# Kernel tuning notes

Hardware: AMD Instinct MI355X
Metric: run time of the kernel (lower is better)

The kernel has to match this reference:

```python
import jax, jax.numpy as jnp
import numpy as np

B = 16384  # batch size
DN = ('NCHW', 'OIHW', 'NCHW')


def maxpool2(x):
    # 2x2 max pool, stride 2, VALID (matches nn.MaxPool2d(2, 2))
    return jax.lax.reduce_window(x, -jnp.inf, jax.lax.max,
                                 (1, 1, 2, 2), (1, 1, 2, 2), 'VALID')


def setup_inputs() -> dict:
    key = jax.random.key(0)
    ks = jax.random.split(key, 7)
    return {
        'x': jax.random.normal(ks[0], (B, 1, 32, 32), jnp.float32),
        'w1': jax.random.normal(ks[1], (6, 1, 5, 5), jnp.float32) * 0.1,
        'w2': jax.random.normal(ks[2], (16, 6, 5, 5), jnp.float32) * 0.1,
        'fw1': jax.random.normal(ks[3], (120, 400), jnp.float32) * 0.05,
        'fw2': jax.random.normal(ks[4], (84, 120), jnp.float32) * 0.05,
        'fc3_w': jax.random.normal(ks[5], (10, 84), jnp.float32) * 0.1,
        'fc3_b': jax.random.normal(ks[6], (10,), jnp.float32) * 0.1,
    }


def reference(x, w1, w2, fw1, fw2, fc3_w, fc3_b):
    # conv1 (no bias in StdConv2D) -> relu -> pool
    h = jax.lax.conv_general_dilated(x, w1, (1, 1), 'VALID', dimension_numbers=DN)
    h = maxpool2(jax.nn.relu(h))                      # [B,6,14,14]
    # conv2 -> relu -> pool
    h = jax.lax.conv_general_dilated(h, w2, (1, 1), 'VALID', dimension_numbers=DN)
    h = maxpool2(jax.nn.relu(h))                      # [B,16,5,5]
    h = h.reshape(h.shape[0], 400)                    # channel-major flatten, as torch view
    # StdFC layers: x @ W.T, no bias
    h = jax.nn.relu(h @ fw1.T)                        # [B,120]
    h = jax.nn.relu(h @ fw2.T)                        # [B,84]
    logits = h @ fc3_w.T + fc3_b                      # nn.Linear fc3 with bias
    return jax.nn.softmax(logits, axis=1)
```

## Files before the change

kernel.cpp:

```cpp
#include <hip/hip_runtime.h>
#include <hip/hip_fp16.h>
#include <math.h>

#define TH 256

typedef __attribute__((ext_vector_type(8))) short short8;
typedef __attribute__((ext_vector_type(4))) float floatx4;

#define P1_S   0
#define X_S    9424
#define P2_S   9424
#define BT_S   12816
#define H1_S   12816
#define H2_S   13904
#define LOG_F  7368
#define W1B_U  7752
#define LDS_F  7904

static __device__ __forceinline__ unsigned short f2bf(float x) {
    union { float f; unsigned u; } v; v.f = x;
    return (unsigned short)((v.u + 0x7FFFu + ((v.u >> 16) & 1u)) >> 16);
}
static __device__ __forceinline__ __half2 uash2(unsigned u) {
    union { unsigned u; __half2 h; } v; v.u = u; return v.h;
}
static __device__ __forceinline__ unsigned bfpack(unsigned hi, unsigned lo) {
    return __builtin_amdgcn_perm(hi, lo, 0x07060302u);
}
static __device__ __forceinline__ short8 load_bf8t(const float* row, int kb, int K) {
    int b0 = (kb + 4 <= K) ? kb : (K - 8);
    int b1 = (kb + 8 <= K) ? (kb + 4) : (K - 8);
    uint4 w0 = *(const uint4*)(row + b0);
    uint4 w1 = *(const uint4*)(row + b1);
    union { int4 i; short8 s; } r;
    r.i.x = (int)bfpack(w0.y, w0.x);
    r.i.y = (int)bfpack(w0.w, w0.z);
    r.i.z = (int)bfpack(w1.y, w1.x);
    r.i.w = (int)bfpack(w1.w, w1.z);
    return r.s;
}

__global__ __launch_bounds__(TH) void lenet_kernel(
    const float* __restrict__ x,
    const float* __restrict__ w1,
    const float* __restrict__ w2g,
    const float* __restrict__ fw1,
    const float* __restrict__ fw2,
    const float* __restrict__ fc3w,
    const float* __restrict__ fc3b,
    float* __restrict__ out)
{
    __shared__ __align__(16) float sf[LDS_F];
    short* sh = (short*)sf;
    unsigned* su = (unsigned*)sf;
    const int* p1i = (const int*)sf;

    const int tid  = threadIdx.x;
    const int blk  = blockIdx.x;
    const int lane = tid & 63;
    const int wid  = tid >> 6;
    const int g    = lane >> 4;
    const int cn   = lane & 15;
    const int pr   = cn & 7;

    for (int sub = 0; sub < 3; ++sub) {
        const int nimg = (sub < 2) ? 3 : 2;
        const float4* xg = (const float4*)(x + ((size_t)blk * 8 + sub * 3) * 1024);
        for (int e = tid; e < nimg * 256; e += TH) {
            float4 v = xg[e];
            int m = e >> 8, rem = e & 255;
            int y = rem >> 3, k4 = rem & 7;
            int off = X_S + m * 1090 + y * 34 + k4 * 4;
            *(__half2*)(sh + off)     = __floats2half2_rn(v.x, v.y);
            *(__half2*)(sh + off + 2) = __floats2half2_rn(v.z, v.w);
        }
        if (sub == 0) {
            for (int e = tid; e < 150; e += TH) {
                __half h = __float2half(w1[e]);
                ((__half2*)(su + W1B_U))[e] = __half2half2(h);
            }
            for (int e = tid; e < 2560; e += TH) {
                int oc = e / 160, kk = e - oc * 160;
                int s = kk >> 5, r = kk & 31;
                float v = 0.f;
                if (r < 30) v = w2g[oc * 150 + (r % 6) * 25 + s * 5 + (r / 6)];
                sh[BT_S + oc * 168 + kk] = (short)f2bf(v);
            }
        }
        __syncthreads();

        const int ntask = nimg * 168;
        for (int t = tid; t < ntask; t += TH) {
            int m = t / 168, r = t - m * 168;
            int c = r % 6, q = r / 6;
            int i = q >> 1, hf = q & 1;
            const __half2* wb = (const __half2*)(su + W1B_U) + c * 25;
            const int xbase = X_S + m * 1090 + hf * 14;

            __half2 acc0[7], acc1[7];
            #pragma unroll
            for (int j = 0; j < 7; ++j) { acc0[j] = uash2(0u); acc1[j] = uash2(0u); }
            __half2 wprev[5];
            #pragma unroll
            for (int tt = 0; tt < 6; ++tt) {
                unsigned u[9];
                const unsigned* rp = (const unsigned*)(sh + xbase + (2 * i + tt) * 34);
                #pragma unroll
                for (int qq = 0; qq < 9; ++qq) u[qq] = rp[qq];
                __half2 p0[9], p1[8];
                #pragma unroll
                for (int qq = 0; qq < 9; ++qq) p0[qq] = uash2(u[qq]);
                #pragma unroll
                for (int qq = 0; qq < 8; ++qq)
                    p1[qq] = uash2(__builtin_amdgcn_perm(u[qq + 1], u[qq], 0x05040302u));

                if (tt < 5) {
                    __half2 wc[5];
                    #pragma unroll
                    for (int kx = 0; kx < 5; ++kx) wc[kx] = wb[tt * 5 + kx];
                    #pragma unroll
                    for (int j = 0; j < 7; ++j) {
                        acc0[j] = __hfma2(p0[j],     wc[0], acc0[j]);
                        acc0[j] = __hfma2(p1[j],     wc[1], acc0[j]);
                        acc0[j] = __hfma2(p0[j + 1], wc[2], acc0[j]);
                        acc0[j] = __hfma2(p1[j + 1], wc[3], acc0[j]);
                        acc0[j] = __hfma2(p0[j + 2], wc[4], acc0[j]);
                    }
                    if (tt >= 1) {
                        #pragma unroll
                        for (int j = 0; j < 7; ++j) {
                            acc1[j] = __hfma2(p0[j],     wprev[0], acc1[j]);
                            acc1[j] = __hfma2(p1[j],     wprev[1], acc1[j]);
                            acc1[j] = __hfma2(p0[j + 1], wprev[2], acc1[j]);
                            acc1[j] = __hfma2(p1[j + 1], wprev[3], acc1[j]);
                            acc1[j] = __hfma2(p0[j + 2], wprev[4], acc1[j]);
                        }
                    }
                    #pragma unroll
                    for (int kx = 0; kx < 5; ++kx) wprev[kx] = wc[kx];
                } else {
                    #pragma unroll
                    for (int j = 0; j < 7; ++j) {
                        acc1[j] = __hfma2(p0[j],     wprev[0], acc1[j]);
                        acc1[j] = __hfma2(p1[j],     wprev[1], acc1[j]);
                        acc1[j] = __hfma2(p0[j + 1], wprev[2], acc1[j]);
                        acc1[j] = __hfma2(p1[j + 1], wprev[3], acc1[j]);
                        acc1[j] = __hfma2(p0[j + 2], wprev[4], acc1[j]);
                    }
                }
            }
            int gi = sub * 3 + m;
            short* dst = sh + P1_S + gi * 1178 + i * 84 + hf * 42 + c;
            #pragma unroll
            for (int j = 0; j < 7; ++j) {
                float a0l = __half2float(__low2half(acc0[j]));
                float a0h = __half2float(__high2half(acc0[j]));
                float a1l = __half2float(__low2half(acc1[j]));
                float a1h = __half2float(__high2half(acc1[j]));
                float v = fmaxf(fmaxf(fmaxf(a0l, a0h), fmaxf(a1l, a1h)), 0.f);
                dst[j * 6] = (short)f2bf(v);
            }
        }
        __syncthreads();
    }

    {
        short8 Breg[5];
        #pragma unroll
        for (int s = 0; s < 5; ++s)
            Breg[s] = *(const short8*)(sh + BT_S + cn * 168 + s * 32 + 8 * g);

        for (int e = tid; e < 8 * 24; e += TH) {
            int im = e / 24;
            sh[P2_S + im * 424 + 400 + (e - im * 24)] = 0;
        }

        for (int w = wid; w < 25; w += 4) {
            int i = w / 5, jx = w - 5 * i;
            floatx4 a00 = {0.f,0.f,0.f,0.f}, a01 = {0.f,0.f,0.f,0.f};
            floatx4 a10 = {0.f,0.f,0.f,0.f}, a11 = {0.f,0.f,0.f,0.f};
            #pragma unroll
            for (int s = 0; s < 5; ++s) {
                #pragma unroll
                for (int dy = 0; dy < 2; ++dy) {
                    #pragma unroll
                    for (int dx = 0; dx < 2; ++dx) {
                        int as = pr * 1178 + (2 * i + dy + s) * 84 + (2 * jx + dx) * 6 + 8 * g;
                        int ai = as >> 1;
                        union { int4 i4; short8 s8; } a;
                        a.i4.x = p1i[ai];     a.i4.y = p1i[ai + 1];
                        a.i4.z = p1i[ai + 2]; a.i4.w = p1i[ai + 3];
                        floatx4* acc = dy == 0 ? (dx == 0 ? &a00 : &a01)
                                               : (dx == 0 ? &a10 : &a11);
                        *acc = __builtin_amdgcn_mfma_f32_16x16x32_bf16(a.s8, Breg[s], *acc, 0, 0, 0);
                    }
                }
            }
            if (g < 2) {
                #pragma unroll
                for (int rg = 0; rg < 4; ++rg) {
                    float v = fmaxf(fmaxf(a00[rg], a01[rg]), fmaxf(a10[rg], a11[rg]));
                    v = fmaxf(v, 0.f);
                    int im = 4 * g + rg;
                    sh[P2_S + im * 424 + cn * 25 + i * 5 + jx] = (short)f2bf(v);
                }
            }
        }
    }
    __syncthreads();

    {
        for (int e = tid; e < 8 * 16; e += TH) {
            int im = e >> 4;
            sh[H1_S + im * 136 + 120 + (e & 15)] = 0;
        }
        for (int nt = wid; nt < 8; nt += 4) {
            floatx4 acc = {0.f,0.f,0.f,0.f};
            int n = nt * 16 + cn;
            const float* wrow = fw1 + (size_t)(n < 120 ? n : 119) * 400;
            for (int ks = 0; ks < 13; ++ks) {
                int kb = ks * 32 + 8 * g;
                short8 b = load_bf8t(wrow, kb, 400);
                short8 a = *(const short8*)(sh + P2_S + pr * 424 + kb);
                acc = __builtin_amdgcn_mfma_f32_16x16x32_bf16(a, b, acc, 0, 0, 0);
            }
            if (g < 2 && n < 120) {
                #pragma unroll
                for (int rg = 0; rg < 4; ++rg)
                    sh[H1_S + (4 * g + rg) * 136 + n] = (short)f2bf(fmaxf(acc[rg], 0.f));
            }
        }
    }
    __syncthreads();

    {
        for (int e = tid; e < 8 * 20; e += TH) {
            int im = e / 20;
            sh[H2_S + im * 104 + 84 + (e - im * 20)] = 0;
        }
        for (int nt = wid; nt < 6; nt += 4) {
            floatx4 acc = {0.f,0.f,0.f,0.f};
            int n = nt * 16 + cn;
            const float* wrow = fw2 + (size_t)(n < 84 ? n : 83) * 120;
            for (int ks = 0; ks < 4; ++ks) {
                int kb = ks * 32 + 8 * g;
                short8 b = load_bf8t(wrow, kb, 120);
                short8 a = *(const short8*)(sh + H1_S + pr * 136 + kb);
                acc = __builtin_amdgcn_mfma_f32_16x16x32_bf16(a, b, acc, 0, 0, 0);
            }
            if (g < 2 && n < 84) {
                #pragma unroll
                for (int rg = 0; rg < 4; ++rg)
                    sh[H2_S + (4 * g + rg) * 104 + n] = (short)f2bf(fmaxf(acc[rg], 0.f));
            }
        }
    }
    __syncthreads();

    if (wid == 0) {
        floatx4 acc = {0.f,0.f,0.f,0.f};
        int n = cn;
        const float* wrow = fc3w + (size_t)(n < 10 ? n : 9) * 84;
        for (int ks = 0; ks < 3; ++ks) {
            int kb = ks * 32 + 8 * g;
            short8 b = load_bf8t(wrow, kb, 84);
            short8 a = *(const short8*)(sh + H2_S + pr * 104 + kb);
            acc = __builtin_amdgcn_mfma_f32_16x16x32_bf16(a, b, acc, 0, 0, 0);
        }
        if (g < 2 && n < 10) {
            float bias = fc3b[n];
            #pragma unroll
            for (int rg = 0; rg < 4; ++rg)
                sf[LOG_F + (4 * g + rg) * 12 + n] = acc[rg] + bias;
        }
    }
    __syncthreads();

    if (tid < 8) {
        const float* lg = sf + LOG_F + tid * 12;
        float mx = lg[0];
        #pragma unroll
        for (int n = 1; n < 10; ++n) mx = fmaxf(mx, lg[n]);
        float e[10]; float sum = 0.f;
        #pragma unroll
        for (int n = 0; n < 10; ++n) { e[n] = expf(lg[n] - mx); sum += e[n]; }
        float inv = 1.f / sum;
        float* op = out + ((size_t)blk * 8 + tid) * 10;
        #pragma unroll
        for (int n = 0; n < 10; ++n) op[n] = e[n] * inv;
    }
}

extern "C" void kernel_launch(void* const* d_in, const int* in_sizes, int n_in,
                              void* d_out, int out_size, void* d_ws, size_t ws_size,
                              hipStream_t stream) {
    const float* x    = (const float*)d_in[0];
    const float* w1   = (const float*)d_in[1];
    const float* w2   = (const float*)d_in[2];
    const float* fw1  = (const float*)d_in[3];
    const float* fw2  = (const float*)d_in[4];
    const float* fc3w = (const float*)d_in[5];
    const float* fc3b = (const float*)d_in[6];
    float* outp = (float*)d_out;

    dim3 grid(16384 / 8), block(TH);
    hipLaunchKernelGGL(lenet_kernel, grid, block, 0, stream,
                       x, w1, w2, fw1, fw2, fc3w, fc3b, outp);
}
```

Before: 84.56 us.

## Prefetch next input batch into registers and halve conv2 MFMA count

Input images for the next sub-batch are loaded from global memory into registers while the current conv1 computes, and staging into LDS is done from those registers. A barrier moves to the start of each sub-iteration to protect the LDS buffer. Conv2 now packs both pooling rows (dy) into the M dimension of the MFMA using lanes 8-15, which halves the MFMA count. The two pooled rows are then reduced with a cross-lane shuffle. This adds register pressure and a shuffle in exchange for hidden load latency and fewer matrix instructions.

```diff
diff --git a/kernel.cpp b/kernel.cpp
--- a/kernel.cpp
+++ b/kernel.cpp
@@ -62,17 +62,28 @@
     const int g    = lane >> 4;
     const int cn   = lane & 15;
     const int pr   = cn & 7;
-
+    const int dyr  = cn >> 3;
+
+    float4 xreg[3];
+    {
+        const float4* xg0 = (const float4*)(x + (size_t)blk * 8 * 1024);
+        #pragma unroll
+        for (int j = 0; j < 3; ++j) { int e = tid + j * TH; if (e < 768) xreg[j] = xg0[e]; }
+    }
     for (int sub = 0; sub < 3; ++sub) {
         const int nimg = (sub < 2) ? 3 : 2;
-        const float4* xg = (const float4*)(x + ((size_t)blk * 8 + sub * 3) * 1024);
-        for (int e = tid; e < nimg * 256; e += TH) {
-            float4 v = xg[e];
-            int m = e >> 8, rem = e & 255;
-            int y = rem >> 3, k4 = rem & 7;
-            int off = X_S + m * 1090 + y * 34 + k4 * 4;
-            *(__half2*)(sh + off)     = __floats2half2_rn(v.x, v.y);
-            *(__half2*)(sh + off + 2) = __floats2half2_rn(v.z, v.w);
+        if (sub) __syncthreads();
+        #pragma unroll
+        for (int j = 0; j < 3; ++j) {
+            int e = tid + j * TH;
+            if (e < nimg * 256) {
+                float4 v = xreg[j];
+                int m = e >> 8, rem = e & 255;
+                int y = rem >> 3, k4 = rem & 7;
+                int off = X_S + m * 1090 + y * 34 + k4 * 4;
+                *(__half2*)(sh + off)     = __floats2half2_rn(v.x, v.y);
+                *(__half2*)(sh + off + 2) = __floats2half2_rn(v.z, v.w);
+            }
         }
         if (sub == 0) {
             for (int e = tid; e < 150; e += TH) {
@@ -88,6 +99,13 @@
             }
         }
         __syncthreads();
+
+        if (sub < 2) {
+            const int nimgn = (sub == 0) ? 3 : 2;
+            const float4* xgn = (const float4*)(x + ((size_t)blk * 8 + (sub + 1) * 3) * 1024);
+            #pragma unroll
+            for (int j = 0; j < 3; ++j) { int e = tid + j * TH; if (e < nimgn * 256) xreg[j] = xgn[e]; }
+        }
 
         const int ntask = nimg * 168;
         for (int t = tid; t < ntask; t += TH) {
@@ -161,8 +179,8 @@
                 dst[j * 6] = (short)f2bf(v);
             }
         }
-        __syncthreads();
-    }
+    }
+    __syncthreads();
 
     {
         short8 Breg[5];
@@ -177,32 +195,27 @@
 
         for (int w = wid; w < 25; w += 4) {
             int i = w / 5, jx = w - 5 * i;
-            floatx4 a00 = {0.f,0.f,0.f,0.f}, a01 = {0.f,0.f,0.f,0.f};
-            floatx4 a10 = {0.f,0.f,0.f,0.f}, a11 = {0.f,0.f,0.f,0.f};
+            floatx4 a0 = {0.f,0.f,0.f,0.f}, a1 = {0.f,0.f,0.f,0.f};
             #pragma unroll
             for (int s = 0; s < 5; ++s) {
                 #pragma unroll
-                for (int dy = 0; dy < 2; ++dy) {
-                    #pragma unroll
-                    for (int dx = 0; dx < 2; ++dx) {
-                        int as = pr * 1178 + (2 * i + dy + s) * 84 + (2 * jx + dx) * 6 + 8 * g;
-                        int ai = as >> 1;
-                        union { int4 i4; short8 s8; } a;
-                        a.i4.x = p1i[ai];     a.i4.y = p1i[ai + 1];
-                        a.i4.z = p1i[ai + 2]; a.i4.w = p1i[ai + 3];
-                        floatx4* acc = dy == 0 ? (dx == 0 ? &a00 : &a01)
-                                               : (dx == 0 ? &a10 : &a11);
-                        *acc = __builtin_amdgcn_mfma_f32_16x16x32_bf16(a.s8, Breg[s], *acc, 0, 0, 0);
-                    }
+                for (int dxp = 0; dxp < 2; ++dxp) {
+                    int as = pr * 1178 + (2 * i + dyr + s) * 84 + (2 * jx + dxp) * 6 + 8 * g;
+                    int ai = as >> 1;
+                    union { int4 i4; short8 s8; } a;
+                    a.i4.x = p1i[ai];     a.i4.y = p1i[ai + 1];
+                    a.i4.z = p1i[ai + 2]; a.i4.w = p1i[ai + 3];
+                    floatx4* acc = dxp == 0 ? &a0 : &a1;
+                    *acc = __builtin_amdgcn_mfma_f32_16x16x32_bf16(a.s8, Breg[s], *acc, 0, 0, 0);
                 }
             }
-            if (g < 2) {
-                #pragma unroll
-                for (int rg = 0; rg < 4; ++rg) {
-                    float v = fmaxf(fmaxf(a00[rg], a01[rg]), fmaxf(a10[rg], a11[rg]));
-                    v = fmaxf(v, 0.f);
+            #pragma unroll
+            for (int rg = 0; rg < 4; ++rg) {
+                float v = fmaxf(a0[rg], a1[rg]);
+                v = fmaxf(v, __shfl_xor(v, 32));
+                if (g < 2) {
                     int im = 4 * g + rg;
-                    sh[P2_S + im * 424 + cn * 25 + i * 5 + jx] = (short)f2bf(v);
+                    sh[P2_S + im * 424 + cn * 25 + i * 5 + jx] = (short)f2bf(fmaxf(v, 0.f));
                 }
             }
         }
```

After: 82.24 us. -2.8%, faster.

## Assign two images per wave to eliminate block barriers and prefetch input

Applied to the files above, without the earlier changes.

Restructures the kernel so each wavefront processes its own two images through all stages, using per-wave LDS regions and no __syncthreads after the weight staging. The next image's input is prefetched into registers while conv1 runs. The aim is to remove block-wide barrier stalls, but MFMA tiles become sparsely used (2 of 16 rows) and FC weight loads are repeated per wave, raising MFMA and global-load work per image.

```diff
diff --git a/kernel.cpp b/kernel.cpp
--- a/kernel.cpp
+++ b/kernel.cpp
@@ -7,15 +7,11 @@
 typedef __attribute__((ext_vector_type(8))) short short8;
 typedef __attribute__((ext_vector_type(4))) float floatx4;
 
-#define P1_S   0
-#define X_S    9424
-#define P2_S   9424
-#define BT_S   12816
-#define H1_S   12816
-#define H2_S   13904
-#define LOG_F  7368
-#define W1B_U  7752
-#define LDS_F  7904
+#define WV_STRIDE 3744
+#define SCR_OFF   2360
+#define BT_S      14976
+#define W1B_U     8832
+#define LDS_F     8984
 
 static __device__ __forceinline__ unsigned short f2bf(float x) {
     union { float f; unsigned u; } v; v.f = x;
@@ -61,72 +57,100 @@
     const int wid  = tid >> 6;
     const int g    = lane >> 4;
     const int cn   = lane & 15;
-    const int pr   = cn & 7;
-
-    for (int sub = 0; sub < 3; ++sub) {
-        const int nimg = (sub < 2) ? 3 : 2;
-        const float4* xg = (const float4*)(x + ((size_t)blk * 8 + sub * 3) * 1024);
-        for (int e = tid; e < nimg * 256; e += TH) {
-            float4 v = xg[e];
-            int m = e >> 8, rem = e & 255;
-            int y = rem >> 3, k4 = rem & 7;
-            int off = X_S + m * 1090 + y * 34 + k4 * 4;
+
+    const int P1w  = wid * WV_STRIDE;
+    const int Xw   = P1w + SCR_OFF;
+    const int P2w  = Xw;
+    const int H1w  = P2w + 848;
+    const int H2w  = H1w + 272;
+    const int LOGf = (H2w + 208) >> 1;
+
+    const size_t imgbase = (size_t)blk * 8 + (size_t)wid * 2;
+
+    float4 xreg[4];
+    {
+        const float4* xg = (const float4*)(x + imgbase * 1024);
+        #pragma unroll
+        for (int j = 0; j < 4; ++j) xreg[j] = xg[lane + j * 64];
+    }
+
+    for (int e = tid; e < 150; e += TH)
+        ((__half2*)(su + W1B_U))[e] = __half2half2(__float2half(w1[e]));
+    for (int e = tid; e < 2560; e += TH) {
+        int oc = e / 160, kk = e - oc * 160;
+        int s = kk >> 5, r = kk & 31;
+        float v = 0.f;
+        if (r < 30) v = w2g[oc * 150 + (r % 6) * 25 + s * 5 + (r / 6)];
+        sh[BT_S + oc * 168 + kk] = (short)f2bf(v);
+    }
+    __syncthreads();
+
+
+    for (int img = 0; img < 2; ++img) {
+        #pragma unroll
+        for (int j = 0; j < 4; ++j) {
+            int e = lane + j * 64;
+            float4 v = xreg[j];
+            int y = e >> 3, k4 = e & 7;
+            int off = Xw + y * 34 + k4 * 4;
             *(__half2*)(sh + off)     = __floats2half2_rn(v.x, v.y);
             *(__half2*)(sh + off + 2) = __floats2half2_rn(v.z, v.w);
         }
-        if (sub == 0) {
-            for (int e = tid; e < 150; e += TH) {
-                __half h = __float2half(w1[e]);
-                ((__half2*)(su + W1B_U))[e] = __half2half2(h);
-            }
-            for (int e = tid; e < 2560; e += TH) {
-                int oc = e / 160, kk = e - oc * 160;
-                int s = kk >> 5, r = kk & 31;
-                float v = 0.f;
-                if (r < 30) v = w2g[oc * 150 + (r % 6) * 25 + s * 5 + (r / 6)];
-                sh[BT_S + oc * 168 + kk] = (short)f2bf(v);
-            }
-        }
-        __syncthreads();
-
-        const int ntask = nimg * 168;
-        for (int t = tid; t < ntask; t += TH) {
-            int m = t / 168, r = t - m * 168;
-            int c = r % 6, q = r / 6;
-            int i = q >> 1, hf = q & 1;
-            const __half2* wb = (const __half2*)(su + W1B_U) + c * 25;
-            const int xbase = X_S + m * 1090 + hf * 14;
-
-            __half2 acc0[7], acc1[7];
+        if (img == 0) {
+            const float4* xg = (const float4*)(x + (imgbase + 1) * 1024);
             #pragma unroll
-            for (int j = 0; j < 7; ++j) { acc0[j] = uash2(0u); acc1[j] = uash2(0u); }
-            __half2 wprev[5];
-            #pragma unroll
-            for (int tt = 0; tt < 6; ++tt) {
-                unsigned u[9];
-                const unsigned* rp = (const unsigned*)(sh + xbase + (2 * i + tt) * 34);
-                #pragma unroll
-                for (int qq = 0; qq < 9; ++qq) u[qq] = rp[qq];
-                __half2 p0[9], p1[8];
-                #pragma unroll
-                for (int qq = 0; qq < 9; ++qq) p0[qq] = uash2(u[qq]);
-                #pragma unroll
-                for (int qq = 0; qq < 8; ++qq)
-                    p1[qq] = uash2(__builtin_amdgcn_perm(u[qq + 1], u[qq], 0x05040302u));
-
-                if (tt < 5) {
-                    __half2 wc[5];
+            for (int j = 0; j < 4; ++j) xreg[j] = xg[lane + j * 64];
+        }
+        for (int p = 0; p < 3; ++p) {
+            int t = p * 64 + lane;
+            if (t < 168) {
+                int c = t % 6, q = t / 6;
+                int i = q >> 1, hf = q & 1;
+                const __half2* wb = (const __half2*)(su + W1B_U) + c * 25;
+                const int xbase = Xw + hf * 14;
+
+                __half2 acc0[7], acc1[7];
+                #pragma unroll
+                for (int j = 0; j < 7; ++j) { acc0[j] = uash2(0u); acc1[j] = uash2(0u); }
+                __half2 wprev[5];
+                #pragma unroll
+                for (int tt = 0; tt < 6; ++tt) {
+                    unsigned u[9];
+                    const unsigned* rp = (const unsigned*)(sh + xbase + (2 * i + tt) * 34);
                     #pragma unroll
-                    for (int kx = 0; kx < 5; ++kx) wc[kx] = wb[tt * 5 + kx];
+                    for (int qq = 0; qq < 9; ++qq) u[qq] = rp[qq];
+                    __half2 p0[9], p1[8];
                     #pragma unroll
-                    for (int j = 0; j < 7; ++j) {
-                        acc0[j] = __hfma2(p0[j],     wc[0], acc0[j]);
-                        acc0[j] = __hfma2(p1[j],     wc[1], acc0[j]);
-                        acc0[j] = __hfma2(p0[j + 1], wc[2], acc0[j]);
-                        acc0[j] = __hfma2(p1[j + 1], wc[3], acc0[j]);
-                        acc0[j] = __hfma2(p0[j + 2], wc[4], acc0[j]);
-                    }
-                    if (tt >= 1) {
+                    for (int qq = 0; qq < 9; ++qq) p0[qq] = uash2(u[qq]);
+                    #pragma unroll
+                    for (int qq = 0; qq < 8; ++qq)
+                        p1[qq] = uash2(__builtin_amdgcn_perm(u[qq + 1], u[qq], 0x05040302u));
+
+                    if (tt < 5) {
+                        __half2 wc[5];
+                        #pragma unroll
+                        for (int kx = 0; kx < 5; ++kx) wc[kx] = wb[tt * 5 + kx];
+                        #pragma unroll
+                        for (int j = 0; j < 7; ++j) {
+                            acc0[j] = __hfma2(p0[j],     wc[0], acc0[j]);
+                            acc0[j] = __hfma2(p1[j],     wc[1], acc0[j]);
+                            acc0[j] = __hfma2(p0[j + 1], wc[2], acc0[j]);
+                            acc0[j] = __hfma2(p1[j + 1], wc[3], acc0[j]);
+                            acc0[j] = __hfma2(p0[j + 2], wc[4], acc0[j]);
+                        }
+                        if (tt >= 1) {
+                            #pragma unroll
+                            for (int j = 0; j < 7; ++j) {
+                                acc1[j] = __hfma2(p0[j],     wprev[0], acc1[j]);
+                                acc1[j] = __hfma2(p1[j],     wprev[1], acc1[j]);
+                                acc1[j] = __hfma2(p0[j + 1], wprev[2], acc1[j]);
+                                acc1[j] = __hfma2(p1[j + 1], wprev[3], acc1[j]);
+                                acc1[j] = __hfma2(p0[j + 2], wprev[4], acc1[j]);
+                            }
+                        }
+                        #pragma unroll
+                        for (int kx = 0; kx < 5; ++kx) wprev[kx] = wc[kx];
+                    } else {
                         #pragma unroll
                         for (int j = 0; j < 7; ++j) {
                             acc1[j] = __hfma2(p0[j],     wprev[0], acc1[j]);
@@ -136,33 +160,24 @@
                             acc1[j] = __hfma2(p0[j + 2], wprev[4], acc1[j]);
                         }
                     }
-                    #pragma unroll
-                    for (int kx = 0; kx < 5; ++kx) wprev[kx] = wc[kx];
-                } else {
-                    #pragma unroll
-                    for (int j = 0; j < 7; ++j) {
-                        acc1[j] = __hfma2(p0[j],     wprev[0], acc1[j]);
-                        acc1[j] = __hfma2(p1[j],     wprev[1], acc1[j]);
-                        acc1[j] = __hfma2(p0[j + 1], wprev[2], acc1[j]);
-                        acc1[j] = __hfma2(p1[j + 1], wprev[3], acc1[j]);
-                        acc1[j] = __hfma2(p0[j + 2], wprev[4], acc1[j]);
-                    }
+                }
+                short* dst = sh + P1w + img * 1178 + i * 84 + hf * 42 + c;
+                #pragma unroll
+                for (int j = 0; j < 7; ++j) {
+                    float a0l = __half2float(__low2half(acc0[j]));
+                    float a0h = __half2float(__high2half(acc0[j]));
+                    float a1l = __half2float(__low2half(acc1[j]));
+                    float a1h = __half2float(__high2half(acc1[j]));
+                    float v = fmaxf(fmaxf(fmaxf(a0l, a0h), fmaxf(a1l, a1h)), 0.f);
+                    dst[j * 6] = (short)f2bf(v);
                 }
             }
-            int gi = sub * 3 + m;
-            short* dst = sh + P1_S + gi * 1178 + i * 84 + hf * 42 + c;
-            #pragma unroll
-            for (int j = 0; j < 7; ++j) {
-                float a0l = __half2float(__low2half(acc0[j]));
-                float a0h = __half2float(__high2half(acc0[j]));
-                float a1l = __half2float(__low2half(acc1[j]));
-                float a1h = __half2float(__high2half(acc1[j]));
-                float v = fmaxf(fmaxf(fmaxf(a0l, a0h), fmaxf(a1l, a1h)), 0.f);
-                dst[j * 6] = (short)f2bf(v);
-            }
-        }
-        __syncthreads();
-    }
+        }
+    }
+
+    if (lane < 48) { int im = lane / 24; sh[P2w + im * 424 + 400 + (lane - im * 24)] = 0; }
+    if (lane < 32) { sh[H1w + (lane >> 4) * 136 + 120 + (lane & 15)] = 0; }
+    if (lane < 40) { int im = lane / 20; sh[H2w + im * 104 + 84 + (lane - im * 20)] = 0; }
 
     {
         short8 Breg[5];
@@ -170,114 +185,86 @@
         for (int s = 0; s < 5; ++s)
             Breg[s] = *(const short8*)(sh + BT_S + cn * 168 + s * 32 + 8 * g);
 
-        for (int e = tid; e < 8 * 24; e += TH) {
-            int im = e / 24;
-            sh[P2_S + im * 424 + 400 + (e - im * 24)] = 0;
-        }
-
-        for (int w = wid; w < 25; w += 4) {
+        const int aimg = cn & 1;
+        const int ady  = (cn >> 1) & 1;
+
+        for (int w = 0; w < 25; ++w) {
             int i = w / 5, jx = w - 5 * i;
-            floatx4 a00 = {0.f,0.f,0.f,0.f}, a01 = {0.f,0.f,0.f,0.f};
-            floatx4 a10 = {0.f,0.f,0.f,0.f}, a11 = {0.f,0.f,0.f,0.f};
+            floatx4 a0 = {0.f,0.f,0.f,0.f}, a1 = {0.f,0.f,0.f,0.f};
             #pragma unroll
             for (int s = 0; s < 5; ++s) {
                 #pragma unroll
-                for (int dy = 0; dy < 2; ++dy) {
-                    #pragma unroll
-                    for (int dx = 0; dx < 2; ++dx) {
-                        int as = pr * 1178 + (2 * i + dy + s) * 84 + (2 * jx + dx) * 6 + 8 * g;
-                        int ai = as >> 1;
-                        union { int4 i4; short8 s8; } a;
-                        a.i4.x = p1i[ai];     a.i4.y = p1i[ai + 1];
-                        a.i4.z = p1i[ai + 2]; a.i4.w = p1i[ai + 3];
-                        floatx4* acc = dy == 0 ? (dx == 0 ? &a00 : &a01)
-                                               : (dx == 0 ? &a10 : &a11);
-                        *acc = __builtin_amdgcn_mfma_f32_16x16x32_bf16(a.s8, Breg[s], *acc, 0, 0, 0);
-                    }
+                for (int dxp = 0; dxp < 2; ++dxp) {
+                    int as = P1w + aimg * 1178 + (2 * i + ady + s) * 84 + (2 * jx + dxp) * 6 + 8 * g;
+                    int ai = as >> 1;
+                    union { int4 i4; short8 s8; } a;
+                    a.i4.x = p1i[ai];     a.i4.y = p1i[ai + 1];
+                    a.i4.z = p1i[ai + 2]; a.i4.w = p1i[ai + 3];
+                    floatx4* acc = dxp == 0 ? &a0 : &a1;
+                    *acc = __builtin_amdgcn_mfma_f32_16x16x32_bf16(a.s8, Breg[s], *acc, 0, 0, 0);
                 }
             }
-            if (g < 2) {
-                #pragma unroll
-                for (int rg = 0; rg < 4; ++rg) {
-                    float v = fmaxf(fmaxf(a00[rg], a01[rg]), fmaxf(a10[rg], a11[rg]));
-                    v = fmaxf(v, 0.f);
-                    int im = 4 * g + rg;
-                    sh[P2_S + im * 424 + cn * 25 + i * 5 + jx] = (short)f2bf(v);
+            if (g == 0) {
+                #pragma unroll
+                for (int im = 0; im < 2; ++im) {
+                    float v = fmaxf(fmaxf(a0[im], a1[im]), fmaxf(a0[im + 2], a1[im + 2]));
+                    sh[P2w + im * 424 + cn * 25 + i * 5 + jx] = (short)f2bf(fmaxf(v, 0.f));
                 }
             }
         }
     }
-    __syncthreads();
+
+    for (int nt = 0; nt < 8; ++nt) {
+        floatx4 acc = {0.f,0.f,0.f,0.f};
+        int n = nt * 16 + cn;
+        const float* wrow = fw1 + (size_t)(n < 120 ? n : 119) * 400;
+        for (int ks = 0; ks < 13; ++ks) {
+            int kb = ks * 32 + 8 * g;
+            short8 b = load_bf8t(wrow, kb, 400);
+            short8 a = *(const short8*)(sh + P2w + (cn & 1) * 424 + kb);
+            acc = __builtin_amdgcn_mfma_f32_16x16x32_bf16(a, b, acc, 0, 0, 0);
+        }
+        if (g == 0 && n < 120) {
+            sh[H1w + n]       = (short)f2bf(fmaxf(acc[0], 0.f));
+            sh[H1w + 136 + n] = (short)f2bf(fmaxf(acc[1], 0.f));
+        }
+    }
+
+    for (int nt = 0; nt < 6; ++nt) {
+        floatx4 acc = {0.f,0.f,0.f,0.f};
+        int n = nt * 16 + cn;
+        const float* wrow = fw2 + (size_t)(n < 84 ? n : 83) * 120;
+        for (int ks = 0; ks < 4; ++ks) {
+            int kb = ks * 32 + 8 * g;
+            short8 b = load_bf8t(wrow, kb, 120);
+            short8 a = *(const short8*)(sh + H1w + (cn & 1) * 136 + kb);
+            acc = __builtin_amdgcn_mfma_f32_16x16x32_bf16(a, b, acc, 0, 0, 0);
+        }
+        if (g == 0 && n < 84) {
+            sh[H2w + n]       = (short)f2bf(fmaxf(acc[0], 0.f));
+            sh[H2w + 104 + n] = (short)f2bf(fmaxf(acc[1], 0.f));
+        }
+    }
 
     {
-        for (int e = tid; e < 8 * 16; e += TH) {
-            int im = e >> 4;
-            sh[H1_S + im * 136 + 120 + (e & 15)] = 0;
-        }
-        for (int nt = wid; nt < 8; nt += 4) {
-            floatx4 acc = {0.f,0.f,0.f,0.f};
-            int n = nt * 16 + cn;
-            const float* wrow = fw1 + (size_t)(n < 120 ? n : 119) * 400;
-            for (int ks = 0; ks < 13; ++ks) {
-                int kb = ks * 32 + 8 * g;
-                short8 b = load_bf8t(wrow, kb, 400);
-                short8 a = *(const short8*)(sh + P2_S + pr * 424 + kb);
-                acc = __builtin_amdgcn_mfma_f32_16x16x32_bf16(a, b, acc, 0, 0, 0);
-            }
-            if (g < 2 && n < 120) {
-                #pragma unroll
-                for (int rg = 0; rg < 4; ++rg)
-                    sh[H1_S + (4 * g + rg) * 136 + n] = (short)f2bf(fmaxf(acc[rg], 0.f));
-            }
-        }
-    }
-    __syncthreads();
-
-    {
-        for (int e = tid; e < 8 * 20; e += TH) {
-            int im = e / 20;
-            sh[H2_S + im * 104 + 84 + (e - im * 20)] = 0;
-        }
-        for (int nt = wid; nt < 6; nt += 4) {
-            floatx4 acc = {0.f,0.f,0.f,0.f};
-            int n = nt * 16 + cn;
-            const float* wrow = fw2 + (size_t)(n < 84 ? n : 83) * 120;
-            for (int ks = 0; ks < 4; ++ks) {
-                int kb = ks * 32 + 8 * g;
-                short8 b = load_bf8t(wrow, kb, 120);
-                short8 a = *(const short8*)(sh + H1_S + pr * 136 + kb);
-                acc = __builtin_amdgcn_mfma_f32_16x16x32_bf16(a, b, acc, 0, 0, 0);
-            }
-            if (g < 2 && n < 84) {
-                #pragma unroll
-                for (int rg = 0; rg < 4; ++rg)
-                    sh[H2_S + (4 * g + rg) * 104 + n] = (short)f2bf(fmaxf(acc[rg], 0.f));
-            }
-        }
-    }
-    __syncthreads();
-
-    if (wid == 0) {
         floatx4 acc = {0.f,0.f,0.f,0.f};
         int n = cn;
         const float* wrow = fc3w + (size_t)(n < 10 ? n : 9) * 84;
         for (int ks = 0; ks < 3; ++ks) {
             int kb = ks * 32 + 8 * g;
             short8 b = load_bf8t(wrow, kb, 84);
-            short8 a = *(const short8*)(sh + H2_S + pr * 104 + kb);
+            short8 a = *(const short8*)(sh + H2w + (cn & 1) * 104 + kb);
             acc = __builtin_amdgcn_mfma_f32_16x16x32_bf16(a, b, acc, 0, 0, 0);
         }
-        if (g < 2 && n < 10) {
+        if (g == 0 && n < 10) {
             float bias = fc3b[n];
-            #pragma unroll
-            for (int rg = 0; rg < 4; ++rg)
-                sf[LOG_F + (4 * g + rg) * 12 + n] = acc[rg] + bias;
-        }
-    }
-    __syncthreads();
-
-    if (tid < 8) {
-        const float* lg = sf + LOG_F + tid * 12;
+            sf[LOGf + n]      = acc[0] + bias;
+            sf[LOGf + 12 + n] = acc[1] + bias;
+        }
+    }
+
+    if (lane < 2) {
+        const float* lg = sf + LOGf + lane * 12;
         float mx = lg[0];
         #pragma unroll
         for (int n = 1; n < 10; ++n) mx = fmaxf(mx, lg[n]);
@@ -285,7 +272,7 @@
         #pragma unroll
         for (int n = 0; n < 10; ++n) { e[n] = expf(lg[n] - mx); sum += e[n]; }
         float inv = 1.f / sum;
-        float* op = out + ((size_t)blk * 8 + tid) * 10;
+        float* op = out + (imgbase + lane) * 10;
         #pragma unroll
         for (int n = 0; n < 10; ++n) op[n] = e[n] * inv;
     }
```

Result: slower. 161.6 us (+91.1%).

## Process 4 images per block and pack pool quadrants into MFMA rows

Applied to the files above, without the earlier changes.

Cuts each block from 8 images to 4, which doubles the grid and roughly halves LDS use, so more blocks can be resident. The conv1 stage drops the three-pass sub-batch loop and its extra barriers, and all x loads are issued up front. In conv2, the four 2x2 pool positions now fill the 16 MFMA rows (4 images × 4 positions), so one MFMA chain replaces four, and the max-pool is done with cross-lane shuffles. The trade-off is that the FC weights and the conv2 weight re-layout are loaded and converted twice as often across the grid.

```diff
diff --git a/kernel.cpp b/kernel.cpp
--- a/kernel.cpp
+++ b/kernel.cpp
@@ -8,14 +8,14 @@
 typedef __attribute__((ext_vector_type(4))) float floatx4;
 
 #define P1_S   0
-#define X_S    9424
-#define P2_S   9424
-#define BT_S   12816
-#define H1_S   12816
-#define H2_S   13904
-#define LOG_F  7368
-#define W1B_U  7752
-#define LDS_F  7904
+#define XS_S   4712
+#define P2_S   4712
+#define BT_S   6408
+#define H1_S   6408
+#define H2_S   6952
+#define LOGFI  3684
+#define W1_U   4536
+#define LDS_F  4688
 
 static __device__ __forceinline__ unsigned short f2bf(float x) {
     union { float f; unsigned u; } v; v.f = x;
@@ -61,84 +61,64 @@
     const int wid  = tid >> 6;
     const int g    = lane >> 4;
     const int cn   = lane & 15;
-    const int pr   = cn & 7;
-
-    for (int sub = 0; sub < 3; ++sub) {
-        const int nimg = (sub < 2) ? 3 : 2;
-        const float4* xg = (const float4*)(x + ((size_t)blk * 8 + sub * 3) * 1024);
-        for (int e = tid; e < nimg * 256; e += TH) {
-            float4 v = xg[e];
+
+    {
+        float4 xreg[4];
+        const float4* xg = (const float4*)(x + (size_t)blk * 4 * 1024);
+        #pragma unroll
+        for (int j = 0; j < 4; ++j) xreg[j] = xg[tid + j * TH];
+        for (int e = tid; e < 150; e += TH)
+            ((__half2*)(su + W1_U))[e] = __half2half2(__float2half(w1[e]));
+        #pragma unroll
+        for (int j = 0; j < 4; ++j) {
+            int e = tid + j * TH;
             int m = e >> 8, rem = e & 255;
             int y = rem >> 3, k4 = rem & 7;
-            int off = X_S + m * 1090 + y * 34 + k4 * 4;
+            int off = XS_S + m * 1090 + y * 34 + k4 * 4;
+            float4 v = xreg[j];
             *(__half2*)(sh + off)     = __floats2half2_rn(v.x, v.y);
             *(__half2*)(sh + off + 2) = __floats2half2_rn(v.z, v.w);
         }
-        if (sub == 0) {
-            for (int e = tid; e < 150; e += TH) {
-                __half h = __float2half(w1[e]);
-                ((__half2*)(su + W1B_U))[e] = __half2half2(h);
-            }
-            for (int e = tid; e < 2560; e += TH) {
-                int oc = e / 160, kk = e - oc * 160;
-                int s = kk >> 5, r = kk & 31;
-                float v = 0.f;
-                if (r < 30) v = w2g[oc * 150 + (r % 6) * 25 + s * 5 + (r / 6)];
-                sh[BT_S + oc * 168 + kk] = (short)f2bf(v);
-            }
-        }
-        __syncthreads();
-
-        const int ntask = nimg * 168;
-        for (int t = tid; t < ntask; t += TH) {
-            int m = t / 168, r = t - m * 168;
-            int c = r % 6, q = r / 6;
-            int i = q >> 1, hf = q & 1;
-            const __half2* wb = (const __half2*)(su + W1B_U) + c * 25;
-            const int xbase = X_S + m * 1090 + hf * 14;
-
-            __half2 acc0[7], acc1[7];
-            #pragma unroll
-            for (int j = 0; j < 7; ++j) { acc0[j] = uash2(0u); acc1[j] = uash2(0u); }
-            __half2 wprev[5];
-            #pragma unroll
-            for (int tt = 0; tt < 6; ++tt) {
-                unsigned u[9];
-                const unsigned* rp = (const unsigned*)(sh + xbase + (2 * i + tt) * 34);
-                #pragma unroll
-                for (int qq = 0; qq < 9; ++qq) u[qq] = rp[qq];
-                __half2 p0[9], p1[8];
-                #pragma unroll
-                for (int qq = 0; qq < 9; ++qq) p0[qq] = uash2(u[qq]);
-                #pragma unroll
-                for (int qq = 0; qq < 8; ++qq)
-                    p1[qq] = uash2(__builtin_amdgcn_perm(u[qq + 1], u[qq], 0x05040302u));
-
-                if (tt < 5) {
-                    __half2 wc[5];
-                    #pragma unroll
-                    for (int kx = 0; kx < 5; ++kx) wc[kx] = wb[tt * 5 + kx];
-                    #pragma unroll
-                    for (int j = 0; j < 7; ++j) {
-                        acc0[j] = __hfma2(p0[j],     wc[0], acc0[j]);
-                        acc0[j] = __hfma2(p1[j],     wc[1], acc0[j]);
-                        acc0[j] = __hfma2(p0[j + 1], wc[2], acc0[j]);
-                        acc0[j] = __hfma2(p1[j + 1], wc[3], acc0[j]);
-                        acc0[j] = __hfma2(p0[j + 2], wc[4], acc0[j]);
-                    }
-                    if (tt >= 1) {
-                        #pragma unroll
-                        for (int j = 0; j < 7; ++j) {
-                            acc1[j] = __hfma2(p0[j],     wprev[0], acc1[j]);
-                            acc1[j] = __hfma2(p1[j],     wprev[1], acc1[j]);
-                            acc1[j] = __hfma2(p0[j + 1], wprev[2], acc1[j]);
-                            acc1[j] = __hfma2(p1[j + 1], wprev[3], acc1[j]);
-                            acc1[j] = __hfma2(p0[j + 2], wprev[4], acc1[j]);
-                        }
-                    }
-                    #pragma unroll
-                    for (int kx = 0; kx < 5; ++kx) wprev[kx] = wc[kx];
-                } else {
+    }
+    __syncthreads();
+
+    for (int t = tid; t < 672; t += TH) {
+        int m = t / 168, r = t - m * 168;
+        int c = r % 6, q = r / 6;
+        int i = q >> 1, hf = q & 1;
+        const __half2* wb = (const __half2*)(su + W1_U) + c * 25;
+        const int xbase = XS_S + m * 1090 + hf * 14;
+
+        __half2 acc0[7], acc1[7];
+        #pragma unroll
+        for (int j = 0; j < 7; ++j) { acc0[j] = uash2(0u); acc1[j] = uash2(0u); }
+        __half2 wprev[5];
+        #pragma unroll
+        for (int tt = 0; tt < 6; ++tt) {
+            unsigned u[9];
+            const unsigned* rp = (const unsigned*)(sh + xbase + (2 * i + tt) * 34);
+            #pragma unroll
+            for (int qq = 0; qq < 9; ++qq) u[qq] = rp[qq];
+            __half2 p0[9], p1[8];
+            #pragma unroll
+            for (int qq = 0; qq < 9; ++qq) p0[qq] = uash2(u[qq]);
+            #pragma unroll
+            for (int qq = 0; qq < 8; ++qq)
+                p1[qq] = uash2(__builtin_amdgcn_perm(u[qq + 1], u[qq], 0x05040302u));
+
+            if (tt < 5) {
+                __half2 wc[5];
+                #pragma unroll
+                for (int kx = 0; kx < 5; ++kx) wc[kx] = wb[tt * 5 + kx];
+                #pragma unroll
+                for (int j = 0; j < 7; ++j) {
+                    acc0[j] = __hfma2(p0[j],     wc[0], acc0[j]);
+                    acc0[j] = __hfma2(p1[j],     wc[1], acc0[j]);
+                    acc0[j] = __hfma2(p0[j + 1], wc[2], acc0[j]);
+                    acc0[j] = __hfma2(p1[j + 1], wc[3], acc0[j]);
+                    acc0[j] = __hfma2(p0[j + 2], wc[4], acc0[j]);
+                }
+                if (tt >= 1) {
                     #pragma unroll
                     for (int j = 0; j < 7; ++j) {
                         acc1[j] = __hfma2(p0[j],     wprev[0], acc1[j]);
@@ -148,136 +128,142 @@
                         acc1[j] = __hfma2(p0[j + 2], wprev[4], acc1[j]);
                     }
                 }
+                #pragma unroll
+                for (int kx = 0; kx < 5; ++kx) wprev[kx] = wc[kx];
+            } else {
+                #pragma unroll
+                for (int j = 0; j < 7; ++j) {
+                    acc1[j] = __hfma2(p0[j],     wprev[0], acc1[j]);
+                    acc1[j] = __hfma2(p1[j],     wprev[1], acc1[j]);
+                    acc1[j] = __hfma2(p0[j + 1], wprev[2], acc1[j]);
+                    acc1[j] = __hfma2(p1[j + 1], wprev[3], acc1[j]);
+                    acc1[j] = __hfma2(p0[j + 2], wprev[4], acc1[j]);
+                }
             }
-            int gi = sub * 3 + m;
-            short* dst = sh + P1_S + gi * 1178 + i * 84 + hf * 42 + c;
-            #pragma unroll
-            for (int j = 0; j < 7; ++j) {
-                float a0l = __half2float(__low2half(acc0[j]));
-                float a0h = __half2float(__high2half(acc0[j]));
-                float a1l = __half2float(__low2half(acc1[j]));
-                float a1h = __half2float(__high2half(acc1[j]));
-                float v = fmaxf(fmaxf(fmaxf(a0l, a0h), fmaxf(a1l, a1h)), 0.f);
-                dst[j * 6] = (short)f2bf(v);
-            }
-        }
-        __syncthreads();
-    }
+        }
+        short* dst = sh + P1_S + m * 1178 + i * 84 + hf * 42 + c;
+        #pragma unroll
+        for (int j = 0; j < 7; ++j) {
+            float a0l = __half2float(__low2half(acc0[j]));
+            float a0h = __half2float(__high2half(acc0[j]));
+            float a1l = __half2float(__low2half(acc1[j]));
+            float a1h = __half2float(__high2half(acc1[j]));
+            float v = fmaxf(fmaxf(fmaxf(a0l, a0h), fmaxf(a1l, a1h)), 0.f);
+            dst[j * 6] = (short)f2bf(v);
+        }
+    }
+    __syncthreads();
+
+    for (int e = tid; e < 2560; e += TH) {
+        int oc = e / 160, kk = e - oc * 160;
+        int s = kk >> 5, r = kk & 31;
+        float v = 0.f;
+        if (r < 30) v = w2g[oc * 150 + (r % 6) * 25 + s * 5 + (r / 6)];
+        sh[BT_S + e] = (short)f2bf(v);
+    }
+    if (tid < 96) {
+        int im = tid / 24;
+        sh[P2_S + im * 424 + 400 + (tid - im * 24)] = 0;
+    }
+    __syncthreads();
 
     {
         short8 Breg[5];
         #pragma unroll
         for (int s = 0; s < 5; ++s)
-            Breg[s] = *(const short8*)(sh + BT_S + cn * 168 + s * 32 + 8 * g);
-
-        for (int e = tid; e < 8 * 24; e += TH) {
-            int im = e / 24;
-            sh[P2_S + im * 424 + 400 + (e - im * 24)] = 0;
-        }
+            Breg[s] = *(const short8*)(sh + BT_S + cn * 160 + s * 32 + 8 * g);
+
+        const int aimg = cn & 3;
+        const int ady  = (cn >> 2) & 1;
+        const int adx  = cn >> 3;
 
         for (int w = wid; w < 25; w += 4) {
             int i = w / 5, jx = w - 5 * i;
-            floatx4 a00 = {0.f,0.f,0.f,0.f}, a01 = {0.f,0.f,0.f,0.f};
-            floatx4 a10 = {0.f,0.f,0.f,0.f}, a11 = {0.f,0.f,0.f,0.f};
+            floatx4 acc = {0.f, 0.f, 0.f, 0.f};
             #pragma unroll
             for (int s = 0; s < 5; ++s) {
-                #pragma unroll
-                for (int dy = 0; dy < 2; ++dy) {
-                    #pragma unroll
-                    for (int dx = 0; dx < 2; ++dx) {
-                        int as = pr * 1178 + (2 * i + dy + s) * 84 + (2 * jx + dx) * 6 + 8 * g;
-                        int ai = as >> 1;
-                        union { int4 i4; short8 s8; } a;
-                        a.i4.x = p1i[ai];     a.i4.y = p1i[ai + 1];
-                        a.i4.z = p1i[ai + 2]; a.i4.w = p1i[ai + 3];
-                        floatx4* acc = dy == 0 ? (dx == 0 ? &a00 : &a01)
-                                               : (dx == 0 ? &a10 : &a11);
-                        *acc = __builtin_amdgcn_mfma_f32_16x16x32_bf16(a.s8, Breg[s], *acc, 0, 0, 0);
-                    }
-                }
+                int as = aimg * 1178 + (2 * i + ady + s) * 84 + (2 * jx + adx) * 6 + 8 * g;
+                int ai = as >> 1;
+                union { int4 i4; short8 s8; } a;
+                a.i4.x = p1i[ai];     a.i4.y = p1i[ai + 1];
+                a.i4.z = p1i[ai + 2]; a.i4.w = p1i[ai + 3];
+                acc = __builtin_amdgcn_mfma_f32_16x16x32_bf16(a.s8, Breg[s], acc, 0, 0, 0);
             }
-            if (g < 2) {
-                #pragma unroll
-                for (int rg = 0; rg < 4; ++rg) {
-                    float v = fmaxf(fmaxf(a00[rg], a01[rg]), fmaxf(a10[rg], a11[rg]));
-                    v = fmaxf(v, 0.f);
-                    int im = 4 * g + rg;
-                    sh[P2_S + im * 424 + cn * 25 + i * 5 + jx] = (short)f2bf(v);
-                }
+            #pragma unroll
+            for (int rg = 0; rg < 4; ++rg) {
+                float v = acc[rg];
+                v = fmaxf(v, __shfl_xor(v, 16));
+                v = fmaxf(v, __shfl_xor(v, 32));
+                if (g == 0)
+                    sh[P2_S + rg * 424 + cn * 25 + i * 5 + jx] = (short)f2bf(fmaxf(v, 0.f));
             }
         }
     }
     __syncthreads();
 
-    {
-        for (int e = tid; e < 8 * 16; e += TH) {
-            int im = e >> 4;
-            sh[H1_S + im * 136 + 120 + (e & 15)] = 0;
-        }
-        for (int nt = wid; nt < 8; nt += 4) {
-            floatx4 acc = {0.f,0.f,0.f,0.f};
-            int n = nt * 16 + cn;
-            const float* wrow = fw1 + (size_t)(n < 120 ? n : 119) * 400;
-            for (int ks = 0; ks < 13; ++ks) {
-                int kb = ks * 32 + 8 * g;
-                short8 b = load_bf8t(wrow, kb, 400);
-                short8 a = *(const short8*)(sh + P2_S + pr * 424 + kb);
-                acc = __builtin_amdgcn_mfma_f32_16x16x32_bf16(a, b, acc, 0, 0, 0);
-            }
-            if (g < 2 && n < 120) {
-                #pragma unroll
-                for (int rg = 0; rg < 4; ++rg)
-                    sh[H1_S + (4 * g + rg) * 136 + n] = (short)f2bf(fmaxf(acc[rg], 0.f));
-            }
-        }
-    }
-    __syncthreads();
-
-    {
-        for (int e = tid; e < 8 * 20; e += TH) {
-            int im = e / 20;
-            sh[H2_S + im * 104 + 84 + (e - im * 20)] = 0;
-        }
-        for (int nt = wid; nt < 6; nt += 4) {
-            floatx4 acc = {0.f,0.f,0.f,0.f};
-            int n = nt * 16 + cn;
-            const float* wrow = fw2 + (size_t)(n < 84 ? n : 83) * 120;
-            for (int ks = 0; ks < 4; ++ks) {
-                int kb = ks * 32 + 8 * g;
-                short8 b = load_bf8t(wrow, kb, 120);
-                short8 a = *(const short8*)(sh + H1_S + pr * 136 + kb);
-                acc = __builtin_amdgcn_mfma_f32_16x16x32_bf16(a, b, acc, 0, 0, 0);
-            }
-            if (g < 2 && n < 84) {
-                #pragma unroll
-                for (int rg = 0; rg < 4; ++rg)
-                    sh[H2_S + (4 * g + rg) * 104 + n] = (short)f2bf(fmaxf(acc[rg], 0.f));
-            }
+    if (tid < 64)  sh[H1_S + (tid >> 4) * 136 + 120 + (tid & 15)] = 0;
+    if (tid >= 64 && tid < 144) {
+        int e = tid - 64, im = e / 20;
+        sh[H2_S + im * 104 + 84 + (e - im * 20)] = 0;
+    }
+
+    for (int nt = wid; nt < 8; nt += 4) {
+        floatx4 acc = {0.f, 0.f, 0.f, 0.f};
+        int n = nt * 16 + cn;
+        const float* wrow = fw1 + (size_t)(n < 120 ? n : 119) * 400;
+        for (int ks = 0; ks < 13; ++ks) {
+            int kb = ks * 32 + 8 * g;
+            short8 b = load_bf8t(wrow, kb, 400);
+            short8 a = *(const short8*)(sh + P2_S + (cn & 3) * 424 + kb);
+            acc = __builtin_amdgcn_mfma_f32_16x16x32_bf16(a, b, acc, 0, 0, 0);
+        }
+        if (g == 0 && n < 120) {
+            #pragma unroll
+            for (int rg = 0; rg < 4; ++rg)
+                sh[H1_S + rg * 136 + n] = (short)f2bf(fmaxf(acc[rg], 0.f));
+        }
+    }
+    __syncthreads();
+
+    for (int nt = wid; nt < 6; nt += 4) {
+        floatx4 acc = {0.f, 0.f, 0.f, 0.f};
+        int n = nt * 16 + cn;
+        const float* wrow = fw2 + (size_t)(n < 84 ? n : 83) * 120;
+        for (int ks = 0; ks < 4; ++ks) {
+            int kb = ks * 32 + 8 * g;
+            short8 b = load_bf8t(wrow, kb, 120);
+            short8 a = *(const short8*)(sh + H1_S + (cn & 3) * 136 + kb);
+            acc = __builtin_amdgcn_mfma_f32_16x16x32_bf16(a, b, acc, 0, 0, 0);
+        }
+        if (g == 0 && n < 84) {
+            #pragma unroll
+            for (int rg = 0; rg < 4; ++rg)
+                sh[H2_S + rg * 104 + n] = (short)f2bf(fmaxf(acc[rg], 0.f));
         }
     }
     __syncthreads();
 
     if (wid == 0) {
-        floatx4 acc = {0.f,0.f,0.f,0.f};
+        floatx4 acc = {0.f, 0.f, 0.f, 0.f};
         int n = cn;
         const float* wrow = fc3w + (size_t)(n < 10 ? n : 9) * 84;
         for (int ks = 0; ks < 3; ++ks) {
             int kb = ks * 32 + 8 * g;
             short8 b = load_bf8t(wrow, kb, 84);
-            short8 a = *(const short8*)(sh + H2_S + pr * 104 + kb);
+            short8 a = *(const short8*)(sh + H2_S + (cn & 3) * 104 + kb);
             acc = __builtin_amdgcn_mfma_f32_16x16x32_bf16(a, b, acc, 0, 0, 0);
         }
-        if (g < 2 && n < 10) {
+        if (g == 0 && n < 10) {
             float bias = fc3b[n];
             #pragma unroll
             for (int rg = 0; rg < 4; ++rg)
-                sf[LOG_F + (4 * g + rg) * 12 + n] = acc[rg] + bias;
-        }
-    }
-    __syncthreads();
-
-    if (tid < 8) {
-        const float* lg = sf + LOG_F + tid * 12;
+                sf[LOGFI + rg * 12 + n] = acc[rg] + bias;
+        }
+    }
+    __syncthreads();
+
+    if (tid < 4) {
+        const float* lg = sf + LOGFI + tid * 12;
         float mx = lg[0];
         #pragma unroll
         for (int n = 1; n < 10; ++n) mx = fmaxf(mx, lg[n]);
@@ -285,7 +271,7 @@
         #pragma unroll
         for (int n = 0; n < 10; ++n) { e[n] = expf(lg[n] - mx); sum += e[n]; }
         float inv = 1.f / sum;
-        float* op = out + ((size_t)blk * 8 + tid) * 10;
+        float* op = out + ((size_t)blk * 4 + tid) * 10;
         #pragma unroll
         for (int n = 0; n < 10; ++n) op[n] = e[n] * inv;
     }
@@ -303,7 +289,7 @@
     const float* fc3b = (const float*)d_in[6];
     float* outp = (float*)d_out;
 
-    dim3 grid(16384 / 8), block(TH);
+    dim3 grid(16384 / 4), block(TH);
     hipLaunchKernelGGL(lenet_kernel, grid, block, 0, stream,
                        x, w1, w2, fw1, fw2, fc3w, fc3b, outp);
 }
```

Result: slower. 126.5 us (+49.6%).
